# Kernel optimization log

Measured on AMD Instinct MI355X. Metric: run time of the kernel, lower is better.

## Reference

```python
import jax, jax.numpy as jnp
import numpy as np

B, N, T, E, R, NSEL = 128, 1000, 50, 32000, 4, 500
F0, CF = 3, 20
FS = 2 * CF + F0  # 43


def _conv(x, w, b):
    # NCHW valid conv, stride 1
    y = jax.lax.conv_general_dilated(x, w, (1, 1), 'VALID',
                                     dimension_numbers=('NCHW', 'OIHW', 'NCHW'))
    return y + b[None, :, None, None]


def setup_inputs() -> dict:
    key = jax.random.key(0)
    ks = jax.random.split(key, 20)
    s = 0.1
    return {
        'observation': jax.random.normal(ks[0], (B, F0, N, T), jnp.float32),
        'last_action': jax.random.uniform(ks[1], (B, NSEL + 1), jnp.float32),
        'w_s1': jax.random.normal(ks[2], (3, 3, 1, 3), jnp.float32) * s,
        'b_s1': jax.random.normal(ks[3], (3,), jnp.float32) * s,
        'w_s2': jax.random.normal(ks[4], (20, 3, 1, 48), jnp.float32) * s,
        'b_s2': jax.random.normal(ks[5], (20,), jnp.float32) * s,
        'w_m1': jax.random.normal(ks[6], (3, 3, 1, 21), jnp.float32) * s,
        'b_m1': jax.random.normal(ks[7], (3,), jnp.float32) * s,
        'w_m2': jax.random.normal(ks[8], (20, 3, 1, 30), jnp.float32) * s,
        'b_m2': jax.random.normal(ks[9], (20,), jnp.float32) * s,
        'w_rel': jax.random.normal(ks[10], (R, FS, FS), jnp.float32) * s,
        'w_root': jax.random.normal(ks[11], (FS, FS), jnp.float32) * s,
        'b_g': jax.random.normal(ks[12], (FS,), jnp.float32) * s,
        'w_fin': jax.random.normal(ks[13], (1, 2 * FS + 1, 1, 1), jnp.float32) * s,
        'b_fin': jax.random.normal(ks[14], (1,), jnp.float32) * s,
        'edge_index': jax.random.randint(ks[15], (2, E), 0, N, jnp.int64) if jax.config.jax_enable_x64 else jax.random.randint(ks[15], (2, E), 0, N).astype(jnp.int32),
        'edge_type': jax.random.randint(ks[16], (E,), 0, R).astype(jnp.int32),
        'nodes_to_select': jnp.sort(jax.random.randint(ks[17], (NSEL,), 0, N)).astype(jnp.int32),
    }


def reference(observation, last_action, w_s1, b_s1, w_s2, b_s2, w_m1, b_m1,
              w_m2, b_m2, w_rel, w_root, b_g, w_fin, b_fin,
              edge_index, edge_type, nodes_to_select):
    # temporal feature extraction
    short = jax.nn.relu(_conv(jax.nn.relu(_conv(observation, w_s1, b_s1)), w_s2, b_s2))
    mid = jax.nn.relu(_conv(jax.nn.relu(_conv(observation, w_m1, b_m1)), w_m2, b_m2))
    long = jax.nn.relu(jnp.max(observation, axis=3, keepdims=True))
    temporal = jnp.concatenate([short, mid, long], axis=1)  # [B, 43, N, 1]

    x = temporal[:, :, :, 0].transpose(0, 2, 1)  # [B, N, F]

    # RGCNConv with per-relation mean aggregation
    src, dst = edge_index[0], edge_index[1]
    xw = jnp.einsum('bnf,rfg->bnrg', x, w_rel)        # [B, N, R, F]
    msgs = xw[:, src, edge_type, :]                   # [B, E, F] gather
    seg = dst * R + edge_type                         # per (node, relation) segment
    agg = jax.vmap(lambda m: jax.ops.segment_sum(m, seg, num_segments=N * R))(msgs)
    cnt = jax.ops.segment_sum(jnp.ones((E,), x.dtype), seg, num_segments=N * R)
    inv = jnp.where(cnt > 0, 1.0 / cnt, 0.0)
    agg = (agg * inv[None, :, None]).reshape(B, N, R, FS).sum(axis=2)
    gout = jax.nn.leaky_relu(agg + x @ w_root + b_g, 0.01)  # [B, N, F]

    graph_features = gout.transpose(0, 2, 1)[..., None]     # [B, F, N, 1]
    feat = jnp.concatenate([temporal, graph_features], axis=1)  # [B, 86, N, 1]
    feat = feat[:, :, nodes_to_select, :]                       # [B, 86, NSEL, 1]
    last_stocks = last_action[:, 1:].reshape(B, 1, NSEL, 1)
    feat = jnp.concatenate([last_stocks, feat], axis=1)         # [B, 87, NSEL, 1]

    o = jnp.einsum('bcn,oc->bon', feat[..., 0], w_fin[:, :, 0, 0]) + b_fin[None, :, None]
    o = jnp.concatenate([jnp.zeros((B, 1, 1), o.dtype), o], axis=2)[:, 0, :]  # [B, NSEL+1]
    return jax.nn.softmax(o / 1.0, axis=-1)
```

## Files before the change

### kernel.cpp

```cpp
#include <hip/hip_runtime.h>
#include <hip/hip_fp16.h>
#include <math.h>

#define Bn 128
#define Nn 1000
#define Tn 50
#define En 32000
#define Rn 4
#define FSn 43
#define NSELn 500
#define NFtot (Nn * FSn)

__global__ __launch_bounds__(512) void k_temporal(
    const float* __restrict__ obs,
    const float* __restrict__ w_s1, const float* __restrict__ b_s1,
    const float* __restrict__ w_s2, const float* __restrict__ b_s2,
    const float* __restrict__ w_m1, const float* __restrict__ b_m1,
    const float* __restrict__ w_m2, const float* __restrict__ b_m2,
    float* __restrict__ x)
{
    __shared__ float lds[3 * 64 * 51];

    const int b     = blockIdx.x;
    const int tile0 = blockIdx.y * 64;
    const int tid   = threadIdx.x;
    const int lane  = tid & 63;
    const int w     = __builtin_amdgcn_readfirstlane(tid >> 6);
    const int nrows = (Nn - tile0) < 64 ? (Nn - tile0) : 64;

    for (int c = 0; c < 3; ++c) {
        const float* srcp = obs + ((size_t)(b * 3 + c) * Nn + tile0) * Tn;
        for (int idx = tid; idx < nrows * Tn; idx += 512) {
            const int r = idx / Tn;
            const int t = idx - r * Tn;
            lds[(c * 64 + r) * 51 + t] = srcp[idx];
        }
    }
    __syncthreads();

    float acc[20];
    float mx0 = -1e30f, mx1 = -1e30f, mx2 = -1e30f;

    if (w < 3) {
        #pragma unroll
        for (int o = 0; o < 20; ++o) acc[o] = (w == 0) ? b_s2[o] : 0.f;

        const float s10 = b_s1[0], s11 = b_s1[1], s12 = b_s1[2];
        const int t0 = w * 16;

        #pragma unroll 1
        for (int t = t0; t < t0 + 16; ++t) {
            float ov[9];
            #pragma unroll
            for (int c = 0; c < 3; ++c)
                #pragma unroll
                for (int d = 0; d < 3; ++d)
                    ov[c * 3 + d] = lds[(c * 64 + lane) * 51 + t + d];

            float v0 = s10, v1 = s11, v2 = s12;
            #pragma unroll
            for (int c = 0; c < 3; ++c) {
                v0 += ov[c * 3 + 0] * w_s1[(0 * 3 + c) * 3 + 0]
                    + ov[c * 3 + 1] * w_s1[(0 * 3 + c) * 3 + 1]
                    + ov[c * 3 + 2] * w_s1[(0 * 3 + c) * 3 + 2];
                v1 += ov[c * 3 + 0] * w_s1[(1 * 3 + c) * 3 + 0]
                    + ov[c * 3 + 1] * w_s1[(1 * 3 + c) * 3 + 1]
                    + ov[c * 3 + 2] * w_s1[(1 * 3 + c) * 3 + 2];
                v2 += ov[c * 3 + 0] * w_s1[(2 * 3 + c) * 3 + 0]
                    + ov[c * 3 + 1] * w_s1[(2 * 3 + c) * 3 + 1]
                    + ov[c * 3 + 2] * w_s1[(2 * 3 + c) * 3 + 2];
            }
            v0 = fmaxf(v0, 0.f); v1 = fmaxf(v1, 0.f); v2 = fmaxf(v2, 0.f);
            #pragma unroll
            for (int o = 0; o < 20; ++o) {
                acc[o] += v0 * w_s2[(o * 3 + 0) * 48 + t]
                        + v1 * w_s2[(o * 3 + 1) * 48 + t]
                        + v2 * w_s2[(o * 3 + 2) * 48 + t];
            }
        }

        const int rb0 = (0 * 64 + lane) * 51;
        const int rb1 = (1 * 64 + lane) * 51;
        const int rb2 = (2 * 64 + lane) * 51;
        const int l0 = (w == 0) ? 0 : (w == 1) ? 17 : 34;
        const int l1 = (w == 0) ? 17 : (w == 1) ? 34 : 50;
        #pragma unroll 1
        for (int t = l0; t < l1; ++t) {
            mx0 = fmaxf(mx0, lds[rb0 + t]);
            mx1 = fmaxf(mx1, lds[rb1 + t]);
            mx2 = fmaxf(mx2, lds[rb2 + t]);
        }
    } else {
        #pragma unroll
        for (int o = 0; o < 20; ++o) acc[o] = (w == 3) ? b_m2[o] : 0.f;

        const float m10 = b_m1[0], m11 = b_m1[1], m12 = b_m1[2];
        const int t0 = (w - 3) * 6;

        #pragma unroll 1
        for (int t = t0; t < t0 + 6; ++t) {
            float v0 = m10, v1 = m11, v2 = m12;
            #pragma unroll
            for (int c = 0; c < 3; ++c) {
                const int base = (c * 64 + lane) * 51 + t;
                #pragma unroll
                for (int d = 0; d < 21; ++d) {
                    const float ov = lds[base + d];
                    v0 += ov * w_m1[(0 * 3 + c) * 21 + d];
                    v1 += ov * w_m1[(1 * 3 + c) * 21 + d];
                    v2 += ov * w_m1[(2 * 3 + c) * 21 + d];
                }
            }
            v0 = fmaxf(v0, 0.f); v1 = fmaxf(v1, 0.f); v2 = fmaxf(v2, 0.f);
            #pragma unroll
            for (int o = 0; o < 20; ++o) {
                acc[o] += v0 * w_m2[(o * 3 + 0) * 30 + t]
                        + v1 * w_m2[(o * 3 + 1) * 30 + t]
                        + v2 * w_m2[(o * 3 + 2) * 30 + t];
            }
        }
    }

    __syncthreads();
    if (w == 1 || w == 2) {
        float* r = lds + (w - 1) * 1472 + lane;
        #pragma unroll
        for (int o = 0; o < 20; ++o) r[o * 64] = acc[o];
        r[20 * 64] = mx0;
        r[21 * 64] = mx1;
        r[22 * 64] = mx2;
    } else if (w >= 4) {
        float* r = lds + 2944 + (w - 4) * 1280 + lane;
        #pragma unroll
        for (int o = 0; o < 20; ++o) r[o * 64] = acc[o];
    }
    __syncthreads();

    if (lane < nrows) {
        float* xp = x + ((size_t)b * Nn + tile0 + lane) * FSn;
        if (w == 0) {
            #pragma unroll
            for (int o = 0; o < 20; ++o) {
                const int a = o * 64 + lane;
                xp[o] = fmaxf(acc[o] + lds[a] + lds[1472 + a], 0.f);
            }
            {
                const int a0 = 20 * 64 + lane, a1 = 21 * 64 + lane, a2 = 22 * 64 + lane;
                xp[40] = fmaxf(fmaxf(mx0, fmaxf(lds[a0], lds[1472 + a0])), 0.f);
                xp[41] = fmaxf(fmaxf(mx1, fmaxf(lds[a1], lds[1472 + a1])), 0.f);
                xp[42] = fmaxf(fmaxf(mx2, fmaxf(lds[a2], lds[1472 + a2])), 0.f);
            }
        } else if (w == 3) {
            #pragma unroll
            for (int o = 0; o < 20; ++o) {
                const int a = 2944 + o * 64 + lane;
                xp[20 + o] = fmaxf(acc[o] + lds[a] + lds[a + 1280]
                                          + lds[a + 2560] + lds[a + 3840], 0.f);
            }
        }
    }
}

__global__ __launch_bounds__(256) void k_transpose(const float* __restrict__ x,
                                                   __half* __restrict__ xT)
{
    __shared__ float tile[64][129];
    const int c0  = blockIdx.x * 64;
    const int tid = threadIdx.x;

    const int j  = tid & 63;
    const int bs = tid >> 6;
    for (int bb = bs; bb < Bn; bb += 4) {
        int c = c0 + j;
        if (c < NFtot) tile[j][bb] = x[(size_t)bb * NFtot + c];
    }
    __syncthreads();

    const int b  = tid & 127;
    for (int jj = (tid >> 7); jj < 64; jj += 2) {
        int c = c0 + jj;
        if (c < NFtot) xT[(size_t)c * Bn + b] = __float2half(tile[jj][b]);
    }
}

__global__ void k_zero(int* __restrict__ cnt, int* __restrict__ pos)
{
    int i = blockIdx.x * blockDim.x + threadIdx.x;
    if (i < 4096) { cnt[i] = 0; pos[i] = 0; }
}

__global__ void k_count(const int* __restrict__ ei, const int* __restrict__ et,
                        int* __restrict__ cnt)
{
    int e = blockIdx.x * blockDim.x + threadIdx.x;
    if (e < En) {
        int dst = ei[En + e];
        atomicAdd(&cnt[dst * Rn + et[e]], 1);
    }
}

__global__ __launch_bounds__(1024) void k_scan(const int* __restrict__ cnt,
                                               int* __restrict__ off)
{
    __shared__ int sums[1024];
    int tid = threadIdx.x;
    int base = tid * 4;
    int c[4];
    int ts = 0;
    #pragma unroll
    for (int k = 0; k < 4; ++k) {
        int i = base + k;
        c[k] = (i < Nn * Rn) ? cnt[i] : 0;
        ts += c[k];
    }
    sums[tid] = ts;
    __syncthreads();
    for (int d = 1; d < 1024; d <<= 1) {
        int t = 0;
        if (tid >= d) t = sums[tid - d];
        __syncthreads();
        sums[tid] += t;
        __syncthreads();
    }
    int excl = sums[tid] - ts;
    #pragma unroll
    for (int k = 0; k < 4; ++k) {
        int i = base + k;
        off[i] = excl;
        excl += c[k];
    }
}

__global__ void k_fill(const int* __restrict__ ei, const int* __restrict__ et,
                       const int* __restrict__ off, int* __restrict__ pos,
                       int* __restrict__ csr)
{
    int e = blockIdx.x * blockDim.x + threadIdx.x;
    if (e < En) {
        int src = ei[e];
        int dst = ei[En + e];
        int seg = dst * Rn + et[e];
        int p = atomicAdd(&pos[seg], 1);
        csr[off[seg] + p] = src;
    }
}

__global__ __launch_bounds__(256) void k_agg4(
    const __half* __restrict__ xT,
    const int* __restrict__ csr, const int* __restrict__ off,
    const int* __restrict__ cnt, const int* __restrict__ sel,
    __half* __restrict__ abar)
{
    __shared__ int srcs[128];

    const int blk = blockIdx.x;
    const int i   = blk >> 2;
    const int r   = blk & 3;
    const int dst = sel[i];
    const int tid = threadIdx.x;
    const int b4  = tid & 31;
    const int fc  = tid >> 5;

    const int seg = dst * Rn + r;
    const int c   = cnt[seg];
    const int o   = off[seg];
    const int cc  = (c < 128) ? c : 128;
    if (tid < cc) srcs[tid] = csr[o + tid];
    __syncthreads();

    const int nk = (fc < 3) ? 6 : 5;

    float4 acc[6];
    #pragma unroll
    for (int k = 0; k < 6; ++k) acc[k] = make_float4(0.f, 0.f, 0.f, 0.f);

    const float2* xT2 = (const float2*)xT;
    for (int j = 0; j < cc; ++j) {
        const int src = srcs[j];
        const float2* base = xT2 + (size_t)src * (FSn * 32) + (size_t)fc * 32 + b4;
        #pragma unroll
        for (int k = 0; k < 6; ++k) {
            if (k < nk) {
                float2 raw = base[k * 8 * 32];
                const __half2 h0 = ((const __half2*)&raw)[0];
                const __half2 h1 = ((const __half2*)&raw)[1];
                const float2 f0 = __half22float2(h0);
                const float2 f1 = __half22float2(h1);
                acc[k].x += f0.x; acc[k].y += f0.y;
                acc[k].z += f1.x; acc[k].w += f1.y;
            }
        }
    }

    const float inv = (c > 0) ? 1.f / (float)c : 0.f;
    float2* ab2 = (float2*)abar + (size_t)(i * Rn + r) * (FSn * 32) + (size_t)fc * 32 + b4;
    #pragma unroll
    for (int k = 0; k < 6; ++k) {
        if (k < nk) {
            float2 st;
            ((__half2*)&st)[0] = __floats2half2_rn(acc[k].x * inv, acc[k].y * inv);
            ((__half2*)&st)[1] = __floats2half2_rn(acc[k].z * inv, acc[k].w * inv);
            ab2[k * 8 * 32] = st;
        }
    }
}

__global__ __launch_bounds__(512) void k_trans(
    const __half* __restrict__ xT, const __half* __restrict__ abar,
    const float* __restrict__ w_rel, const float* __restrict__ w_root,
    const float* __restrict__ b_g,
    const float* __restrict__ w_fin, const float* __restrict__ b_fin,
    const float* __restrict__ la,
    const int* __restrict__ sel,
    float* __restrict__ logitT)
{
    __shared__ float red[FSn + 1][Bn];

    const int i   = blockIdx.x;
    const int dst = sel[i];
    const int tid = threadIdx.x;
    const int fs  = tid >> 7;
    const int b   = tid & 127;

    const int f0 = fs * 11;
    const int nf = (fs == 3) ? 10 : 11;

    float a[5][11];
    #pragma unroll
    for (int rr = 0; rr < 4; ++rr) {
        const __half* ap = abar + ((size_t)(i * Rn + rr) * FSn + f0) * Bn + b;
        #pragma unroll
        for (int k = 0; k < 11; ++k)
            a[rr][k] = (k < nf) ? __half2float(ap[(size_t)k * Bn]) : 0.f;
    }
    {
        const __half* xp = xT + ((size_t)dst * FSn + f0) * Bn + b;
        #pragma unroll
        for (int k = 0; k < 11; ++k)
            a[4][k] = (k < nf) ? __half2float(xp[(size_t)k * Bn]) : 0.f;
    }

    float accg[FSn];
    #pragma unroll
    for (int g = 0; g < FSn; ++g) accg[g] = 0.f;
    float psum = 0.f;

    #pragma unroll
    for (int k = 0; k < 11; ++k) {
        if (k < nf) {
            const int f = f0 + k;
            #pragma unroll
            for (int rr = 0; rr < 5; ++rr) {
                const float av = a[rr][k];
                const float* wrow = (rr < 4)
                    ? (w_rel + ((size_t)rr * FSn + f) * FSn)
                    : (w_root + (size_t)f * FSn);
                #pragma unroll
                for (int g = 0; g < FSn; ++g) accg[g] += av * wrow[g];
            }
            psum += a[4][k] * w_fin[1 + f];
        }
    }

    if (fs == 3) {
        #pragma unroll
        for (int g = 0; g < FSn; ++g) red[g][b] = accg[g];
        red[FSn][b] = psum;
    }
    __syncthreads();
    if (fs == 2) {
        #pragma unroll
        for (int g = 0; g < FSn; ++g) red[g][b] += accg[g];
        red[FSn][b] += psum;
    }
    __syncthreads();
    if (fs == 1) {
        #pragma unroll
        for (int g = 0; g < FSn; ++g) red[g][b] += accg[g];
        red[FSn][b] += psum;
    }
    __syncthreads();
    if (fs == 0) {
        float logit = b_fin[0] + w_fin[0] * la[(size_t)b * (NSELn + 1) + 1 + i]
                    + psum + red[FSn][b];
        #pragma unroll
        for (int g = 0; g < FSn; ++g) {
            float v = accg[g] + red[g][b] + b_g[g];
            v = (v > 0.f) ? v : 0.01f * v;
            logit += v * w_fin[44 + g];
        }
        logitT[(size_t)i * Bn + b] = logit;
    }
}

__global__ __launch_bounds__(512) void k_softmax(const float* __restrict__ logitT,
                                                 float* __restrict__ out)
{
    __shared__ float red[512];
    const int b   = blockIdx.x;
    const int tid = threadIdx.x;

    const float l = (tid < NSELn) ? logitT[(size_t)tid * Bn + b] : -1e30f;
    red[tid] = l;
    __syncthreads();
    for (int s = 256; s > 0; s >>= 1) {
        if (tid < s) red[tid] = fmaxf(red[tid], red[tid + s]);
        __syncthreads();
    }
    const float m = fmaxf(red[0], 0.f);
    __syncthreads();

    const float e = (tid < NSELn) ? expf(l - m) : 0.f;
    red[tid] = e;
    __syncthreads();
    for (int s = 256; s > 0; s >>= 1) {
        if (tid < s) red[tid] += red[tid + s];
        __syncthreads();
    }
    const float e0  = expf(-m);
    const float inv = 1.f / (red[0] + e0);

    if (tid == 0) out[(size_t)b * (NSELn + 1)] = e0 * inv;
    if (tid < NSELn) out[(size_t)b * (NSELn + 1) + 1 + tid] = e * inv;
}

extern "C" void kernel_launch(void* const* d_in, const int* in_sizes, int n_in,
                              void* d_out, int out_size, void* d_ws, size_t ws_size,
                              hipStream_t stream)
{
    const float* obs    = (const float*)d_in[0];
    const float* la     = (const float*)d_in[1];
    const float* w_s1   = (const float*)d_in[2];
    const float* b_s1   = (const float*)d_in[3];
    const float* w_s2   = (const float*)d_in[4];
    const float* b_s2   = (const float*)d_in[5];
    const float* w_m1   = (const float*)d_in[6];
    const float* b_m1   = (const float*)d_in[7];
    const float* w_m2   = (const float*)d_in[8];
    const float* b_m2   = (const float*)d_in[9];
    const float* w_rel  = (const float*)d_in[10];
    const float* w_root = (const float*)d_in[11];
    const float* b_g    = (const float*)d_in[12];
    const float* w_fin  = (const float*)d_in[13];
    const float* b_fin  = (const float*)d_in[14];
    const int*   ei     = (const int*)d_in[15];
    const int*   et     = (const int*)d_in[16];
    const int*   sel    = (const int*)d_in[17];
    float*       out    = (float*)d_out;

    char* wsb     = (char*)d_ws;
    float* x      = (float*)wsb;
    __half* abar  = (__half*)wsb;
    __half* xTh   = (__half*)(wsb + 22016000);
    int*   cnt    = (int*)(wsb + 33024000);
    int*   offb   = cnt + 4096;
    int*   pos    = offb + 4096;
    int*   csr    = pos + 4096;
    float* logitT = (float*)(csr + 32000);

    hipLaunchKernelGGL(k_zero,  dim3(16),  dim3(256), 0, stream, cnt, pos);
    hipLaunchKernelGGL(k_count, dim3((En + 255) / 256), dim3(256), 0, stream, ei, et, cnt);
    hipLaunchKernelGGL(k_scan,  dim3(1),   dim3(1024), 0, stream, cnt, offb);
    hipLaunchKernelGGL(k_fill,  dim3((En + 255) / 256), dim3(256), 0, stream, ei, et, offb, pos, csr);

    hipLaunchKernelGGL(k_temporal, dim3(Bn, (Nn + 63) / 64), dim3(512), 0, stream,
                       obs, w_s1, b_s1, w_s2, b_s2, w_m1, b_m1, w_m2, b_m2, x);

    hipLaunchKernelGGL(k_transpose, dim3((NFtot + 63) / 64), dim3(256), 0, stream, x, xTh);

    hipLaunchKernelGGL(k_agg4, dim3(NSELn * Rn), dim3(256), 0, stream,
                       xTh, csr, offb, cnt, sel, abar);

    hipLaunchKernelGGL(k_trans, dim3(NSELn), dim3(512), 0, stream,
                       xTh, abar, w_rel, w_root, b_g, w_fin, b_fin, la, sel, logitT);

    hipLaunchKernelGGL(k_softmax, dim3(Bn), dim3(512), 0, stream, logitT, out);
}
```

Baseline: 239.6 us.

## Fuse neighbor aggregation into graph transform kernel via shared memory

Merges the per-(node,relation) mean aggregation kernel into the relational transform kernel. Each block now gathers all four relations' neighbor features into LDS as half precision and consumes them directly, removing the global abar round-trip and one launch. It also splits the mid-conv inner sum into partial accumulators to shorten the dependency chain. The trade-off is fewer blocks (500 instead of 2000) doing the gather, each with more registers, which may reduce latency hiding.

```diff
diff --git a/kernel.cpp b/kernel.cpp
--- a/kernel.cpp
+++ b/kernel.cpp
@@ -103,13 +103,15 @@
             #pragma unroll
             for (int c = 0; c < 3; ++c) {
                 const int base = (c * 64 + lane) * 51 + t;
+                float p0 = 0.f, p1 = 0.f, p2 = 0.f;
                 #pragma unroll
                 for (int d = 0; d < 21; ++d) {
                     const float ov = lds[base + d];
-                    v0 += ov * w_m1[(0 * 3 + c) * 21 + d];
-                    v1 += ov * w_m1[(1 * 3 + c) * 21 + d];
-                    v2 += ov * w_m1[(2 * 3 + c) * 21 + d];
+                    p0 += ov * w_m1[(0 * 3 + c) * 21 + d];
+                    p1 += ov * w_m1[(1 * 3 + c) * 21 + d];
+                    p2 += ov * w_m1[(2 * 3 + c) * 21 + d];
                 }
+                v0 += p0; v1 += p1; v2 += p2;
             }
             v0 = fmaxf(v0, 0.f); v1 = fmaxf(v1, 0.f); v2 = fmaxf(v2, 0.f);
             #pragma unroll
@@ -245,93 +247,93 @@
     }
 }
 
-__global__ __launch_bounds__(256) void k_agg4(
+__global__ __launch_bounds__(512) void k_graph(
     const __half* __restrict__ xT,
-    const int* __restrict__ csr, const int* __restrict__ off,
-    const int* __restrict__ cnt, const int* __restrict__ sel,
-    __half* __restrict__ abar)
-{
-    __shared__ int srcs[128];
-
-    const int blk = blockIdx.x;
-    const int i   = blk >> 2;
-    const int r   = blk & 3;
-    const int dst = sel[i];
-    const int tid = threadIdx.x;
-    const int b4  = tid & 31;
-    const int fc  = tid >> 5;
-
-    const int seg = dst * Rn + r;
-    const int c   = cnt[seg];
-    const int o   = off[seg];
-    const int cc  = (c < 128) ? c : 128;
-    if (tid < cc) srcs[tid] = csr[o + tid];
-    __syncthreads();
-
-    const int nk = (fc < 3) ? 6 : 5;
-
-    float4 acc[6];
-    #pragma unroll
-    for (int k = 0; k < 6; ++k) acc[k] = make_float4(0.f, 0.f, 0.f, 0.f);
-
-    const float2* xT2 = (const float2*)xT;
-    for (int j = 0; j < cc; ++j) {
-        const int src = srcs[j];
-        const float2* base = xT2 + (size_t)src * (FSn * 32) + (size_t)fc * 32 + b4;
-        #pragma unroll
-        for (int k = 0; k < 6; ++k) {
-            if (k < nk) {
-                float2 raw = base[k * 8 * 32];
-                const __half2 h0 = ((const __half2*)&raw)[0];
-                const __half2 h1 = ((const __half2*)&raw)[1];
-                const float2 f0 = __half22float2(h0);
-                const float2 f1 = __half22float2(h1);
-                acc[k].x += f0.x; acc[k].y += f0.y;
-                acc[k].z += f1.x; acc[k].w += f1.y;
-            }
-        }
-    }
-
-    const float inv = (c > 0) ? 1.f / (float)c : 0.f;
-    float2* ab2 = (float2*)abar + (size_t)(i * Rn + r) * (FSn * 32) + (size_t)fc * 32 + b4;
-    #pragma unroll
-    for (int k = 0; k < 6; ++k) {
-        if (k < nk) {
-            float2 st;
-            ((__half2*)&st)[0] = __floats2half2_rn(acc[k].x * inv, acc[k].y * inv);
-            ((__half2*)&st)[1] = __floats2half2_rn(acc[k].z * inv, acc[k].w * inv);
-            ab2[k * 8 * 32] = st;
-        }
-    }
-}
-
-__global__ __launch_bounds__(512) void k_trans(
-    const __half* __restrict__ xT, const __half* __restrict__ abar,
     const float* __restrict__ w_rel, const float* __restrict__ w_root,
     const float* __restrict__ b_g,
     const float* __restrict__ w_fin, const float* __restrict__ b_fin,
     const float* __restrict__ la,
-    const int* __restrict__ sel,
+    const int* __restrict__ csr, const int* __restrict__ off,
+    const int* __restrict__ cnt, const int* __restrict__ sel,
     float* __restrict__ logitT)
 {
-    __shared__ float red[FSn + 1][Bn];
+    __shared__ __align__(16) char smem[44032 + 2048 + 32];
+    __half* ab    = (__half*)smem;
+    int*    srcs  = (int*)(smem + 44032);
+    int*    scnt  = (int*)(smem + 44032 + 2048);
+    int*    tcnt  = scnt + 4;
+    float*  red   = (float*)smem;
 
     const int i   = blockIdx.x;
     const int dst = sel[i];
     const int tid = threadIdx.x;
-    const int fs  = tid >> 7;
-    const int b   = tid & 127;
-
+
+    {
+        const int r = tid >> 7;
+        const int j = tid & 127;
+        const int c = cnt[dst * Rn + r];
+        const int o = off[dst * Rn + r];
+        if (j == 0) { tcnt[r] = c; scnt[r] = (c < 128) ? c : 128; }
+        if (j < c && j < 128) srcs[r * 128 + j] = csr[o + j];
+    }
+    __syncthreads();
+
+    {
+        const int r  = tid >> 7;
+        const int fc = (tid >> 5) & 3;
+        const int b4 = tid & 31;
+        const int nk = (fc < 3) ? 11 : 10;
+
+        float4 acc[11];
+        #pragma unroll
+        for (int k = 0; k < 11; ++k) acc[k] = make_float4(0.f, 0.f, 0.f, 0.f);
+
+        const int cc = scnt[r];
+        const float2* xT2 = (const float2*)xT;
+        for (int j = 0; j < cc; ++j) {
+            const int src = srcs[r * 128 + j];
+            const float2* base = xT2 + (size_t)src * (FSn * 32) + (size_t)fc * 32 + b4;
+            #pragma unroll
+            for (int k = 0; k < 11; ++k) {
+                if (k < nk) {
+                    float2 raw = base[(size_t)k * 4 * 32];
+                    const __half2 h0 = ((const __half2*)&raw)[0];
+                    const __half2 h1 = ((const __half2*)&raw)[1];
+                    const float2 f0 = __half22float2(h0);
+                    const float2 f1 = __half22float2(h1);
+                    acc[k].x += f0.x; acc[k].y += f0.y;
+                    acc[k].z += f1.x; acc[k].w += f1.y;
+                }
+            }
+        }
+
+        const int  tc  = tcnt[r];
+        const float inv = (tc > 0) ? 1.f / (float)tc : 0.f;
+        float2* ab2 = (float2*)ab;
+        #pragma unroll
+        for (int k = 0; k < 11; ++k) {
+            if (k < nk) {
+                const int f = fc + 4 * k;
+                float2 st;
+                ((__half2*)&st)[0] = __floats2half2_rn(acc[k].x * inv, acc[k].y * inv);
+                ((__half2*)&st)[1] = __floats2half2_rn(acc[k].z * inv, acc[k].w * inv);
+                ab2[(r * FSn + f) * 32 + b4] = st;
+            }
+        }
+    }
+    __syncthreads();
+
+    const int fs = tid >> 7;
+    const int b  = tid & 127;
     const int f0 = fs * 11;
     const int nf = (fs == 3) ? 10 : 11;
 
     float a[5][11];
     #pragma unroll
     for (int rr = 0; rr < 4; ++rr) {
-        const __half* ap = abar + ((size_t)(i * Rn + rr) * FSn + f0) * Bn + b;
         #pragma unroll
         for (int k = 0; k < 11; ++k)
-            a[rr][k] = (k < nf) ? __half2float(ap[(size_t)k * Bn]) : 0.f;
+            a[rr][k] = (k < nf) ? __half2float(ab[(rr * FSn + f0 + k) * Bn + b]) : 0.f;
     }
     {
         const __half* xp = xT + ((size_t)dst * FSn + f0) * Bn + b;
@@ -362,30 +364,32 @@
         }
     }
 
+    __syncthreads();
+
     if (fs == 3) {
         #pragma unroll
-        for (int g = 0; g < FSn; ++g) red[g][b] = accg[g];
-        red[FSn][b] = psum;
+        for (int g = 0; g < FSn; ++g) red[g * Bn + b] = accg[g];
+        red[FSn * Bn + b] = psum;
     }
     __syncthreads();
     if (fs == 2) {
         #pragma unroll
-        for (int g = 0; g < FSn; ++g) red[g][b] += accg[g];
-        red[FSn][b] += psum;
+        for (int g = 0; g < FSn; ++g) red[g * Bn + b] += accg[g];
+        red[FSn * Bn + b] += psum;
     }
     __syncthreads();
     if (fs == 1) {
         #pragma unroll
-        for (int g = 0; g < FSn; ++g) red[g][b] += accg[g];
-        red[FSn][b] += psum;
+        for (int g = 0; g < FSn; ++g) red[g * Bn + b] += accg[g];
+        red[FSn * Bn + b] += psum;
     }
     __syncthreads();
     if (fs == 0) {
         float logit = b_fin[0] + w_fin[0] * la[(size_t)b * (NSELn + 1) + 1 + i]
-                    + psum + red[FSn][b];
+                    + psum + red[FSn * Bn + b];
         #pragma unroll
         for (int g = 0; g < FSn; ++g) {
-            float v = accg[g] + red[g][b] + b_g[g];
+            float v = accg[g] + red[g * Bn + b] + b_g[g];
             v = (v > 0.f) ? v : 0.01f * v;
             logit += v * w_fin[44 + g];
         }
@@ -450,7 +454,6 @@
 
     char* wsb     = (char*)d_ws;
     float* x      = (float*)wsb;
-    __half* abar  = (__half*)wsb;
     __half* xTh   = (__half*)(wsb + 22016000);
     int*   cnt    = (int*)(wsb + 33024000);
     int*   offb   = cnt + 4096;
@@ -468,11 +471,9 @@
 
     hipLaunchKernelGGL(k_transpose, dim3((NFtot + 63) / 64), dim3(256), 0, stream, x, xTh);
 
-    hipLaunchKernelGGL(k_agg4, dim3(NSELn * Rn), dim3(256), 0, stream,
-                       xTh, csr, offb, cnt, sel, abar);
-
-    hipLaunchKernelGGL(k_trans, dim3(NSELn), dim3(512), 0, stream,
-                       xTh, abar, w_rel, w_root, b_g, w_fin, b_fin, la, sel, logitT);
+    hipLaunchKernelGGL(k_graph, dim3(NSELn), dim3(512), 0, stream,
+                       xTh, w_rel, w_root, b_g, w_fin, b_fin, la,
+                       csr, offb, cnt, sel, logitT);
 
     hipLaunchKernelGGL(k_softmax, dim3(Bn), dim3(512), 0, stream, logitT, out);
 }
```

New measurement: 235.9 us. No clear change (-1.5%).
